# Optimization experiments

Hardware: AMD Instinct MI355X
Metric: run time of the kernel (lower is better)

Reference implementation:

```python
import jax, jax.numpy as jnp
import numpy as np

N_NEIGHBORS = 9
MIN_STD, MAX_STD = 0.01, 0.5
EPS = 1e-8


def setup_inputs() -> dict:
    key = jax.random.key(0)
    k1, k2, k3 = jax.random.split(key, 3)
    B, C, H, W = 8, 2048, 28, 28
    M = 8192
    features = jax.random.normal(k1, (B, C, H, W), dtype=jnp.float32)
    memory_bank = jax.random.normal(k2, (M, C), dtype=jnp.float32)
    influence_weight = jnp.ones((C,), dtype=jnp.float32)
    distance_weight = jnp.ones((1,), dtype=jnp.float32)
    noise_unit = jax.random.normal(k3, (B * H * W, C), dtype=jnp.float32)
    return {
        "features": features,
        "memory_bank": memory_bank,
        "influence_weight": influence_weight,
        "distance_weight": distance_weight,
        "noise_unit": noise_unit,
    }


def _std(x, axis=None, keepdims=False):
    # torch.std default: unbiased (ddof=1)
    return jnp.std(x, axis=axis, keepdims=keepdims, ddof=1)


def reference(features, memory_bank, influence_weight, distance_weight, noise_unit):
    B, C, H, W = features.shape
    M = memory_bank.shape[0]
    k = min(N_NEIGHBORS, M)

    # [B*H*W, C]
    f = features.transpose(0, 2, 3, 1).reshape(B * H * W, C)

    # Euclidean cdist via the (||a||^2 + ||b||^2 - 2 a.b) expansion
    f2 = jnp.sum(f * f, axis=1, keepdims=True)            # [N,1]
    m2 = jnp.sum(memory_bank * memory_bank, axis=1)       # [M]
    d2 = f2 + m2[None, :] - 2.0 * (f @ memory_bank.T)     # [N,M]
    dist = jnp.sqrt(jnp.clip(d2, 0.0, None))

    # top-k smallest distances (sorted ascending, like torch.topk largest=False)
    neg_vals, idx = jax.lax.top_k(-dist, k)               # [N,k]
    topk_distances = -neg_vals

    # gather neighbor features and per-dim influence
    nn_feats = memory_bank[idx]                           # [N,k,C]
    influence_scores = jnp.mean(jnp.abs(f[:, None, :] - nn_feats), axis=1)  # [N,C]
    influence_scores = influence_scores * influence_weight[None, :]

    # normalize influence per-row
    influence_norm = influence_scores - jnp.mean(influence_scores, axis=-1, keepdims=True)
    influence_norm = influence_norm / (_std(influence_scores, axis=-1, keepdims=True) + EPS)

    # distance signal: row-mean distance, broadcast to [N,C], global-normalized
    ds = jnp.mean(topk_distances, axis=-1, keepdims=True)  # [N,1]
    ds_e = jnp.broadcast_to(ds, influence_norm.shape)      # [N,C]
    distance_norm = (ds_e - jnp.mean(ds_e)) / (_std(ds_e) + EPS)

    combined = influence_norm + distance_weight * distance_norm
    noise_std = MIN_STD + (MAX_STD - MIN_STD) * jax.nn.sigmoid(combined)  # [N,C]

    noised_flat = f + noise_unit * noise_std
    noised_features = noised_flat.reshape(B, H, W, C).transpose(0, 3, 1, 2)
    influence_map = jnp.mean(influence_scores, axis=-1).reshape(B, H, W)
    noise_std_map = jnp.mean(noise_std, axis=-1).reshape(B, H, W)
    return noised_features, influence_map, noise_std_map
```

## Files before the change

### kernel.cpp

```cpp
#include <hip/hip_runtime.h>
#include <math.h>

typedef __attribute__((ext_vector_type(8))) __bf16 bf16x8;
typedef __attribute__((ext_vector_type(4))) float f32x4;

#define NB 8
#define NC 2048
#define NHW 784
#define NROWS 6272
#define NM 8192
#define NNEI 9
#define NCAND 12
#define NKT 64

static_assert(NROWS == NB * NHW, "dims");

__device__ __forceinline__ unsigned umin32(unsigned a, unsigned b) { return a < b ? a : b; }

__global__ __launch_bounds__(256) void prep_kernel(const float* __restrict__ feat,
                                                   const float* __restrict__ mb,
                                                   float* __restrict__ Af32,
                                                   __bf16* __restrict__ Ahi,
                                                   __bf16* __restrict__ Bhi,
                                                   float* __restrict__ m2) {
  int bid = blockIdx.x;
  int tid = threadIdx.x;
  if (bid < 12800) {
    __shared__ float tile[32][33];
    int b = bid / 1600;
    int c0 = ((bid / 25) & 63) * 32;
    int hw0 = (bid % 25) * 32;
    int tx = tid & 31, ty = tid >> 5;
#pragma unroll
    for (int i = 0; i < 4; ++i) {
      int c = c0 + ty + i * 8;
      int hw = hw0 + tx;
      float v = 0.f;
      if (hw < NHW) v = feat[((size_t)b * NC + c) * NHW + hw];
      tile[ty + i * 8][tx] = v;
    }
    __syncthreads();
#pragma unroll
    for (int i = 0; i < 4; ++i) {
      int hwl = ty + i * 8;
      int hw = hw0 + hwl;
      if (hw < NHW) {
        int n = b * NHW + hw;
        float v = tile[tx][hwl];
        Af32[(size_t)n * NC + c0 + tx] = v;
        Ahi[(size_t)n * NC + c0 + tx] = (__bf16)v;
      }
    }
  } else {
    __shared__ float red[4];
    int m = bid - 12800;
    float ss = 0.f;
#pragma unroll
    for (int i = 0; i < NC / 256; ++i) {
      int c = tid + i * 256;
      float v = mb[(size_t)m * NC + c];
      Bhi[(size_t)m * NC + c] = (__bf16)v;
      ss += v * v;
    }
#pragma unroll
    for (int off = 32; off; off >>= 1) ss += __shfl_xor(ss, off);
    if ((tid & 63) == 0) red[tid >> 6] = ss;
    __syncthreads();
    if (tid == 0) m2[m] = red[0] + red[1] + red[2] + red[3];
  }
}

#define STAGE(SRC, DST) \
  __builtin_amdgcn_global_load_lds((const __attribute__((address_space(1))) void*)(SRC), \
                                   (__attribute__((address_space(3))) void*)(DST), 16, 0, 0)

__global__ __launch_bounds__(512, 2) void gemm8_kernel(const __bf16* __restrict__ Ahi,
                                                       const __bf16* __restrict__ Bhi,
                                                       const float* __restrict__ m2,
                                                       unsigned short* __restrict__ dotq) {
  __shared__ __align__(16) char lds[131072];
  int tid = threadIdx.x;
  int lane = tid & 63, w = tid >> 6;
  int bid = blockIdx.x;
  int r = lane & 15, kq = lane >> 4;
  int r4 = (lane >> 4) * 4, cL = lane & 15;

  if (bid >= 768) {
    int lb = bid - 768;
    size_t m0l = (size_t)(lb & 7) * 1024 + (size_t)(lb >> 3) * 32;
    int n0l = 6144 + w * 16;
    const __bf16* aB = Ahi + (size_t)(n0l + r) * NC + kq * 8;
    const __bf16* bB0 = Bhi + (m0l + r) * NC + kq * 8;
    const __bf16* bB1 = Bhi + (m0l + 16 + r) * NC + kq * 8;
    f32x4 acc0 = {}, acc1 = {};
    bf16x8 a0 = *(const bf16x8*)aB;
    bf16x8 b0 = *(const bf16x8*)bB0;
    bf16x8 b1 = *(const bf16x8*)bB1;
#pragma unroll 4
    for (int kt = 0; kt < NKT; ++kt) {
      int ktn = (kt + 1) & 63;
      bf16x8 an = *(const bf16x8*)(aB + ktn * 32);
      bf16x8 b0n = *(const bf16x8*)(bB0 + ktn * 32);
      bf16x8 b1n = *(const bf16x8*)(bB1 + ktn * 32);
      acc0 = __builtin_amdgcn_mfma_f32_16x16x32_bf16(a0, b0, acc0, 0, 0, 0);
      acc1 = __builtin_amdgcn_mfma_f32_16x16x32_bf16(a0, b1, acc1, 0, 0, 0);
      a0 = an; b0 = b0n; b1 = b1n;
    }
#pragma unroll
    for (int g = 0; g < 2; ++g) {
      float m2g = m2[m0l + g * 16 + cL];
      f32x4 ac = g ? acc1 : acc0;
#pragma unroll
      for (int q = 0; q < 4; ++q) {
        int grow = n0l + r4 + q;
        float sc = m2g - 2.f * ac[q];
        int qi = (int)(sc * 16.f);
        qi = qi < 0 ? 0 : (qi > 65535 ? 65535 : qi);
        dotq[(size_t)grow * NM + (m0l + g * 16 + cL)] = (unsigned short)qi;
      }
    }
    return;
  }

  int xcd = bid & 7, lin = bid >> 3;
  int mt = xcd * 4 + (lin & 3), rtl = lin >> 2;
  size_t n0 = (size_t)rtl * 256, m0 = (size_t)mt * 256;
  int wr = w >> 2, wc = w & 3;

  int p = lane & 3;
  const char* aSrc[2];
  const char* bSrc[2];
  int aDst[2], bDst[2];
#pragma unroll
  for (int j = 0; j < 2; ++j) {
    int rloc = (w * 2 + j) * 16 + (lane >> 2);
    int kqs = (p - (rloc >> 1)) & 3;
    aSrc[j] = (const char*)Ahi + (n0 + rloc) * (NC * 2) + kqs * 16;
    bSrc[j] = (const char*)Bhi + (m0 + rloc) * (NC * 2) + kqs * 16;
    aDst[j] = (w * 2 + j) * 1024;
    bDst[j] = 16384 + (w * 2 + j) * 1024;
  }
  int s16 = (kq + (r >> 1)) & 3;
  int aRd = wr * 8192 + r * 64 + s16 * 16;
  int bRd = 16384 + wc * 4096 + r * 64 + s16 * 16;

  f32x4 acc[8][4] = {};

#pragma unroll
  for (int t = 0; t < 2; ++t) {
    int sb = t * 32768, kb = t * 64;
#pragma unroll
    for (int j = 0; j < 2; ++j)
      STAGE(aSrc[j] + kb, lds + sb + aDst[j]);
#pragma unroll
    for (int j = 0; j < 2; ++j)
      STAGE(bSrc[j] + kb, lds + sb + bDst[j]);
  }
  asm volatile("s_waitcnt vmcnt(4)" ::: "memory");
  __builtin_amdgcn_s_barrier();
  __builtin_amdgcn_sched_barrier(0);

#pragma unroll 4
  for (int kt = 0; kt < NKT; ++kt) {
    int sb = (kt & 3) * 32768;
    int kt2 = (kt + 2) & 63;
    int sb2 = (kt2 & 3) * 32768;
    int kb2 = kt2 * 64;
    bf16x8 av[4], bv[4];
#pragma unroll
    for (int j = 0; j < 2; ++j)
      STAGE(aSrc[j] + kb2, lds + sb2 + aDst[j]);
#pragma unroll
    for (int f = 0; f < 4; ++f) av[f] = *(const bf16x8*)(lds + sb + aRd + f * 1024);
#pragma unroll
    for (int g = 0; g < 4; ++g) bv[g] = *(const bf16x8*)(lds + sb + bRd + g * 1024);
    __builtin_amdgcn_s_setprio(1);
#pragma unroll
    for (int f = 0; f < 4; ++f)
#pragma unroll
      for (int g = 0; g < 4; ++g)
        acc[f][g] = __builtin_amdgcn_mfma_f32_16x16x32_bf16(av[f], bv[g], acc[f][g], 0, 0, 0);
    __builtin_amdgcn_s_setprio(0);
#pragma unroll
    for (int j = 0; j < 2; ++j)
      STAGE(bSrc[j] + kb2, lds + sb2 + bDst[j]);
#pragma unroll
    for (int f = 0; f < 4; ++f) av[f] = *(const bf16x8*)(lds + sb + aRd + (f + 4) * 1024);
    __builtin_amdgcn_s_setprio(1);
#pragma unroll
    for (int f = 0; f < 4; ++f)
#pragma unroll
      for (int g = 0; g < 4; ++g)
        acc[f + 4][g] = __builtin_amdgcn_mfma_f32_16x16x32_bf16(av[f], bv[g], acc[f + 4][g], 0, 0, 0);
    __builtin_amdgcn_s_setprio(0);
    asm volatile("s_waitcnt vmcnt(4)" ::: "memory");
    __builtin_amdgcn_s_barrier();
    __builtin_amdgcn_sched_barrier(0);
  }

  float m2r[4];
#pragma unroll
  for (int g = 0; g < 4; ++g) m2r[g] = m2[m0 + wc * 64 + g * 16 + cL];
#pragma unroll
  for (int f = 0; f < 8; ++f) {
    int grow0 = (int)n0 + wr * 128 + f * 16 + r4;
#pragma unroll
    for (int g = 0; g < 4; ++g) {
      size_t gcol = m0 + wc * 64 + g * 16 + cL;
#pragma unroll
      for (int q = 0; q < 4; ++q) {
        float sc = m2r[g] - 2.f * acc[f][g][q];
        int qi = (int)(sc * 16.f);
        qi = qi < 0 ? 0 : (qi > 65535 ? 65535 : qi);
        dotq[(size_t)(grow0 + q) * NM + gcol] = (unsigned short)qi;
      }
    }
  }
}

__global__ __launch_bounds__(256) void selres_kernel(const unsigned short* __restrict__ dotq,
                                                     const float* __restrict__ Af32,
                                                     const float* __restrict__ mb,
                                                     int* __restrict__ tki,
                                                     float* __restrict__ dsv) {
  __shared__ float fbuf[NC];
  __shared__ unsigned wmin[4];
  __shared__ int cidxL[NCAND];
  __shared__ double d2s[NCAND];
  int n = blockIdx.x;
  int tid = threadIdx.x;
  int lane = tid & 63, w = tid >> 6;

  unsigned kk[32];
  {
    const uint4* dq = (const uint4*)(dotq + (size_t)n * NM + tid * 32);
    unsigned base = tid * 32;
#pragma unroll
    for (int s = 0; s < 4; ++s) {
      uint4 v = dq[s];
      unsigned c0 = v.x, c1 = v.y, c2 = v.z, c3 = v.w;
      kk[s * 8 + 0] = ((c0 & 0xFFFFu) << 13) | (base + s * 8 + 0);
      kk[s * 8 + 1] = ((c0 >> 16) << 13)     | (base + s * 8 + 1);
      kk[s * 8 + 2] = ((c1 & 0xFFFFu) << 13) | (base + s * 8 + 2);
      kk[s * 8 + 3] = ((c1 >> 16) << 13)     | (base + s * 8 + 3);
      kk[s * 8 + 4] = ((c2 & 0xFFFFu) << 13) | (base + s * 8 + 4);
      kk[s * 8 + 5] = ((c2 >> 16) << 13)     | (base + s * 8 + 5);
      kk[s * 8 + 6] = ((c3 & 0xFFFFu) << 13) | (base + s * 8 + 6);
      kk[s * 8 + 7] = ((c3 >> 16) << 13)     | (base + s * 8 + 7);
    }
  }
#pragma unroll
  for (int i = 0; i < NC / 256; ++i)
    fbuf[tid + i * 256] = Af32[(size_t)n * NC + tid + i * 256];

  unsigned lmin = 0xFFFFFFFFu;
#pragma unroll
  for (int i = 0; i < 32; ++i) lmin = umin32(lmin, kk[i]);
  unsigned t = lmin;
#pragma unroll
  for (int off = 32; off; off >>= 1) t = umin32(t, (unsigned)__shfl_xor((int)t, off));
  if (lane == 0) wmin[w] = t;
  __syncthreads();

  for (int r = 0; r < NCAND; ++r) {
    unsigned g = umin32(umin32(wmin[0], wmin[1]), umin32(wmin[2], wmin[3]));
    if (tid == 0) cidxL[r] = (int)(g & 8191u);
    __syncthreads();
    int owner = (int)((g & 8191u) >> 5);
    if ((owner >> 6) == w) {
      if (tid == owner) {
#pragma unroll
        for (int i = 0; i < 32; ++i)
          if (kk[i] == g) kk[i] = 0xFFFFFFFFu;
        lmin = 0xFFFFFFFFu;
#pragma unroll
        for (int i = 0; i < 32; ++i) lmin = umin32(lmin, kk[i]);
      }
      unsigned t2 = lmin;
#pragma unroll
      for (int off = 32; off; off >>= 1) t2 = umin32(t2, (unsigned)__shfl_xor((int)t2, off));
      if (lane == 0) wmin[w] = t2;
    }
    __syncthreads();
  }

#pragma unroll
  for (int jj = 0; jj < 3; ++jj) {
    int j = w * 3 + jj;
    const float* mrow = mb + (size_t)cidxL[j] * NC;
    double acc = 0.0;
#pragma unroll
    for (int i = 0; i < 32; ++i) {
      int c = lane + i * 64;
      double d = (double)fbuf[c] - (double)mrow[c];
      acc += d * d;
    }
#pragma unroll
    for (int off = 32; off; off >>= 1) acc += __shfl_xor(acc, off);
    if (lane == 0) d2s[j] = acc;
  }
  __syncthreads();

  if (tid == 0) {
    double dacc = 0.0;
    bool used[NCAND] = {};
    for (int r = 0; r < NNEI; ++r) {
      int bj = 0; double bv = 1e300; int bidx = 0x7fffffff;
      for (int j = 0; j < NCAND; ++j) {
        if (used[j]) continue;
        if (d2s[j] < bv || (d2s[j] == bv && cidxL[j] < bidx)) { bv = d2s[j]; bidx = cidxL[j]; bj = j; }
      }
      used[bj] = true;
      tki[(size_t)n * NNEI + r] = bidx;
      dacc += sqrt(bv > 0.0 ? bv : 0.0);
    }
    dsv[n] = (float)(dacc * (1.0 / 9.0));
  }
}

__global__ __launch_bounds__(256) void stats_kernel(const float* __restrict__ dsv,
                                                    float* __restrict__ stats) {
  __shared__ float buf[NROWS];
  __shared__ float red[4];
  int tid = threadIdx.x;
  float s = 0.f;
  for (int i = tid; i < NROWS; i += 256) { float v = dsv[i]; buf[i] = v; s += v; }
#pragma unroll
  for (int off = 32; off; off >>= 1) s += __shfl_xor(s, off);
  if ((tid & 63) == 0) red[tid >> 6] = s;
  __syncthreads();
  float mu = (red[0] + red[1] + red[2] + red[3]) * (1.f / NROWS);
  __syncthreads();
  float q = 0.f;
  for (int i = tid; i < NROWS; i += 256) { float d = buf[i] - mu; q += d * d; }
#pragma unroll
  for (int off = 32; off; off >>= 1) q += __shfl_xor(q, off);
  if ((tid & 63) == 0) red[tid >> 6] = q;
  __syncthreads();
  if (tid == 0) {
    float SSb = (red[0] + red[1] + red[2] + red[3]) * (float)NC;
    float var = SSb / ((float)NROWS * (float)NC - 1.f);
    stats[0] = mu;
    stats[1] = 1.f / (sqrtf(var) + 1e-8f);
  }
}

__global__ __launch_bounds__(256) void fuse_kernel(const float* __restrict__ Af32,
                                                   const __bf16* __restrict__ Bhi,
                                                   const float* __restrict__ noise,
                                                   const float* __restrict__ iw,
                                                   const float* __restrict__ dwp,
                                                   const int* __restrict__ topk_idx,
                                                   const float* __restrict__ dsv,
                                                   const float* __restrict__ stats,
                                                   float* __restrict__ noised_tmp,
                                                   float* __restrict__ out_infl,
                                                   float* __restrict__ out_nstd) {
  __shared__ int idx[NNEI];
  __shared__ float red[4];
  int n = blockIdx.x;
  int tid = threadIdx.x;
  if (tid < NNEI) idx[tid] = topk_idx[(size_t)n * NNEI + tid];
  __syncthreads();

  int c0 = tid * 8;
  const float* frow = Af32 + (size_t)n * NC + c0;
  float4 fa = *(const float4*)frow;
  float4 fb = *(const float4*)(frow + 4);
  float f_c[8] = {fa.x, fa.y, fa.z, fa.w, fb.x, fb.y, fb.z, fb.w};
  float a_c[8] = {};
  for (int j = 0; j < NNEI; ++j) {
    bf16x8 mv = *(const bf16x8*)(Bhi + (size_t)idx[j] * NC + c0);
#pragma unroll
    for (int k = 0; k < 8; ++k) a_c[k] += fabsf(f_c[k] - (float)mv[k]);
  }
  float4 w0 = *(const float4*)(iw + c0);
  float4 w1 = *(const float4*)(iw + c0 + 4);
  float wv[8] = {w0.x, w0.y, w0.z, w0.w, w1.x, w1.y, w1.z, w1.w};
  float s_c[8];
  float sum_s = 0.f, sum_s2 = 0.f;
#pragma unroll
  for (int k = 0; k < 8; ++k) {
    float s = (a_c[k] * (1.f / 9.f)) * wv[k];
    s_c[k] = s;
    sum_s += s;
    sum_s2 += s * s;
  }
#pragma unroll
  for (int off = 32; off; off >>= 1) sum_s += __shfl_xor(sum_s, off);
  if ((tid & 63) == 0) red[tid >> 6] = sum_s;
  __syncthreads();
  float tot_s = red[0] + red[1] + red[2] + red[3];
  __syncthreads();
#pragma unroll
  for (int off = 32; off; off >>= 1) sum_s2 += __shfl_xor(sum_s2, off);
  if ((tid & 63) == 0) red[tid >> 6] = sum_s2;
  __syncthreads();
  float tot_s2 = red[0] + red[1] + red[2] + red[3];
  __syncthreads();

  float mu = tot_s * (1.f / NC);
  float var = (tot_s2 - (float)NC * mu * mu) * (1.f / (NC - 1));
  float rstd = 1.f / (sqrtf(fmaxf(var, 0.f)) + 1e-8f);
  float dnorm = (dsv[n] - stats[0]) * stats[1];
  float dwv = dwp[0];

  float4 na = *(const float4*)(noise + (size_t)n * NC + c0);
  float4 nb = *(const float4*)(noise + (size_t)n * NC + c0 + 4);
  float nz[8] = {na.x, na.y, na.z, na.w, nb.x, nb.y, nb.z, nb.w};
  float o[8];
  float nsum = 0.f;
#pragma unroll
  for (int k = 0; k < 8; ++k) {
    float inorm = (s_c[k] - mu) * rstd;
    float comb = inorm + dwv * dnorm;
    float sig = 1.f / (1.f + expf(-comb));
    float nstd = 0.01f + 0.49f * sig;
    nsum += nstd;
    o[k] = f_c[k] + nz[k] * nstd;
  }
  float* orow = noised_tmp + (size_t)n * NC + c0;
  *(float4*)orow = make_float4(o[0], o[1], o[2], o[3]);
  *(float4*)(orow + 4) = make_float4(o[4], o[5], o[6], o[7]);
#pragma unroll
  for (int off = 32; off; off >>= 1) nsum += __shfl_xor(nsum, off);
  if ((tid & 63) == 0) red[tid >> 6] = nsum;
  __syncthreads();
  if (tid == 0) {
    out_infl[n] = tot_s * (1.f / NC);
    out_nstd[n] = (red[0] + red[1] + red[2] + red[3]) * (1.f / NC);
  }
}

__global__ __launch_bounds__(256) void transpose_kernel(const float* __restrict__ src,
                                                        float* __restrict__ dst) {
  __shared__ float tile[32][33];
  int b = blockIdx.z;
  int c0 = blockIdx.y * 32;
  int hw0 = blockIdx.x * 32;
  int tx = threadIdx.x & 31, ty = threadIdx.x >> 5;
#pragma unroll
  for (int i = 0; i < 4; ++i) {
    int hw = hw0 + ty + i * 8;
    if (hw < NHW) tile[ty + i * 8][tx] = src[((size_t)(b * NHW + hw)) * NC + c0 + tx];
  }
  __syncthreads();
#pragma unroll
  for (int i = 0; i < 4; ++i) {
    int c = c0 + ty + i * 8;
    int hw = hw0 + tx;
    if (hw < NHW) dst[((size_t)b * NC + c) * NHW + hw] = tile[tx][ty + i * 8];
  }
}

extern "C" void kernel_launch(void* const* d_in, const int* in_sizes, int n_in,
                              void* d_out, int out_size, void* d_ws, size_t ws_size,
                              hipStream_t stream) {
  (void)in_sizes; (void)n_in; (void)out_size; (void)ws_size;
  const float* feat  = (const float*)d_in[0];
  const float* mb    = (const float*)d_in[1];
  const float* iw    = (const float*)d_in[2];
  const float* dwp   = (const float*)d_in[3];
  const float* noise = (const float*)d_in[4];
  float* out = (float*)d_out;
  float* out_noised = out;
  float* out_infl = out + (size_t)NB * NC * NHW;
  float* out_nstd = out_infl + NROWS;

  char* ws = (char*)d_ws;
  size_t off = 0;
  auto alloc = [&](size_t sz) -> char* {
    char* p = ws + off;
    off += (sz + 255) & ~(size_t)255;
    return p;
  };
  float* Af32 = (float*)alloc((size_t)NROWS * NC * 4);
  __bf16* Ahi = (__bf16*)alloc((size_t)NROWS * NC * 2);
  __bf16* Bhi = (__bf16*)alloc((size_t)NM * NC * 2);
  float* m2v = (float*)alloc((size_t)NM * 4);
  int* tki = (int*)alloc((size_t)NROWS * NNEI * 4);
  float* dsv = (float*)alloc((size_t)NROWS * 4);
  float* stv = (float*)alloc(256);
  unsigned short* dotq = (unsigned short*)alloc((size_t)NROWS * NM * 2);
  float* noised_tmp = (float*)dotq;

  prep_kernel<<<12800 + NM, 256, 0, stream>>>(feat, mb, Af32, Ahi, Bhi, m2v);
  gemm8_kernel<<<1024, 512, 0, stream>>>(Ahi, Bhi, m2v, dotq);
  selres_kernel<<<NROWS, 256, 0, stream>>>(dotq, Af32, mb, tki, dsv);
  stats_kernel<<<1, 256, 0, stream>>>(dsv, stv);
  fuse_kernel<<<NROWS, 256, 0, stream>>>(Af32, Bhi, noise, iw, dwp, tki, dsv, stv,
                                         noised_tmp, out_infl, out_nstd);
  transpose_kernel<<<dim3(25, 64, NB), 256, 0, stream>>>(noised_tmp, out_noised);
}
```

Before: 440.3 us.

## Switch distance GEMM to int8 MFMA with wider candidate re-rank

Quantizes features and memory bank to int8 (scale 20) and runs the candidate-distance GEMM with i32 16x16x64 int8 MFMA, halving the K-loop iterations and the bytes staged through LDS. To make up for the coarser screening, the exact double-precision re-rank now keeps 32 candidates instead of 12. This targets GEMM compute and bandwidth. It adds extra re-rank work and a separate int8 bank copy, and risks missing true neighbours when quantization error pushes them beyond the top 32. Clipping at ±127 (about ±6.35) is normally harmless for normal inputs.

```diff
diff --git a/kernel.cpp b/kernel.cpp
--- a/kernel.cpp
+++ b/kernel.cpp
@@ -3,6 +3,7 @@
 
 typedef __attribute__((ext_vector_type(8))) __bf16 bf16x8;
 typedef __attribute__((ext_vector_type(4))) float f32x4;
+typedef __attribute__((ext_vector_type(4))) int i32x4;
 
 #define NB 8
 #define NC 2048
@@ -10,17 +11,24 @@
 #define NROWS 6272
 #define NM 8192
 #define NNEI 9
-#define NCAND 12
-#define NKT 64
+#define NCAND 32
+#define NKT 32
 
 static_assert(NROWS == NB * NHW, "dims");
 
 __device__ __forceinline__ unsigned umin32(unsigned a, unsigned b) { return a < b ? a : b; }
+
+__device__ __forceinline__ signed char quant20(float v) {
+  int q = (int)rintf(v * 20.f);
+  q = q < -127 ? -127 : (q > 127 ? 127 : q);
+  return (signed char)q;
+}
 
 __global__ __launch_bounds__(256) void prep_kernel(const float* __restrict__ feat,
                                                    const float* __restrict__ mb,
                                                    float* __restrict__ Af32,
-                                                   __bf16* __restrict__ Ahi,
+                                                   signed char* __restrict__ Ai8,
+                                                   signed char* __restrict__ Bi8,
                                                    __bf16* __restrict__ Bhi,
                                                    float* __restrict__ m2) {
   int bid = blockIdx.x;
@@ -48,7 +56,7 @@
         int n = b * NHW + hw;
         float v = tile[tx][hwl];
         Af32[(size_t)n * NC + c0 + tx] = v;
-        Ahi[(size_t)n * NC + c0 + tx] = (__bf16)v;
+        Ai8[(size_t)n * NC + c0 + tx] = quant20(v);
       }
     }
   } else {
@@ -59,6 +67,7 @@
     for (int i = 0; i < NC / 256; ++i) {
       int c = tid + i * 256;
       float v = mb[(size_t)m * NC + c];
+      Bi8[(size_t)m * NC + c] = quant20(v);
       Bhi[(size_t)m * NC + c] = (__bf16)v;
       ss += v * v;
     }
@@ -74,8 +83,8 @@
   __builtin_amdgcn_global_load_lds((const __attribute__((address_space(1))) void*)(SRC), \
                                    (__attribute__((address_space(3))) void*)(DST), 16, 0, 0)
 
-__global__ __launch_bounds__(512, 2) void gemm8_kernel(const __bf16* __restrict__ Ahi,
-                                                       const __bf16* __restrict__ Bhi,
+__global__ __launch_bounds__(512, 2) void gemm8_kernel(const signed char* __restrict__ Ai8,
+                                                       const signed char* __restrict__ Bi8,
                                                        const float* __restrict__ m2,
                                                        unsigned short* __restrict__ dotq) {
   __shared__ __align__(16) char lds[131072];
@@ -89,32 +98,31 @@
     int lb = bid - 768;
     size_t m0l = (size_t)(lb & 7) * 1024 + (size_t)(lb >> 3) * 32;
     int n0l = 6144 + w * 16;
-    const __bf16* aB = Ahi + (size_t)(n0l + r) * NC + kq * 8;
-    const __bf16* bB0 = Bhi + (m0l + r) * NC + kq * 8;
-    const __bf16* bB1 = Bhi + (m0l + 16 + r) * NC + kq * 8;
-    f32x4 acc0 = {}, acc1 = {};
-    bf16x8 a0 = *(const bf16x8*)aB;
-    bf16x8 b0 = *(const bf16x8*)bB0;
-    bf16x8 b1 = *(const bf16x8*)bB1;
+    const signed char* aB = Ai8 + (size_t)(n0l + r) * NC + kq * 16;
+    const signed char* bB0 = Bi8 + (m0l + r) * NC + kq * 16;
+    const signed char* bB1 = Bi8 + (m0l + 16 + r) * NC + kq * 16;
+    i32x4 acc0 = {}, acc1 = {};
+    i32x4 a0 = *(const i32x4*)aB;
+    i32x4 b0 = *(const i32x4*)bB0;
+    i32x4 b1 = *(const i32x4*)bB1;
 #pragma unroll 4
     for (int kt = 0; kt < NKT; ++kt) {
-      int ktn = (kt + 1) & 63;
-      bf16x8 an = *(const bf16x8*)(aB + ktn * 32);
-      bf16x8 b0n = *(const bf16x8*)(bB0 + ktn * 32);
-      bf16x8 b1n = *(const bf16x8*)(bB1 + ktn * 32);
-      acc0 = __builtin_amdgcn_mfma_f32_16x16x32_bf16(a0, b0, acc0, 0, 0, 0);
-      acc1 = __builtin_amdgcn_mfma_f32_16x16x32_bf16(a0, b1, acc1, 0, 0, 0);
+      int ktn = (kt + 1) & 31;
+      i32x4 an = *(const i32x4*)(aB + ktn * 64);
+      i32x4 b0n = *(const i32x4*)(bB0 + ktn * 64);
+      i32x4 b1n = *(const i32x4*)(bB1 + ktn * 64);
+      acc0 = __builtin_amdgcn_mfma_i32_16x16x64_i8(a0, b0, acc0, 0, 0, 0);
+      acc1 = __builtin_amdgcn_mfma_i32_16x16x64_i8(a0, b1, acc1, 0, 0, 0);
       a0 = an; b0 = b0n; b1 = b1n;
     }
 #pragma unroll
     for (int g = 0; g < 2; ++g) {
-      float m2g = m2[m0l + g * 16 + cL];
-      f32x4 ac = g ? acc1 : acc0;
+      float m2g16 = m2[m0l + g * 16 + cL] * 16.f;
+      i32x4 ac = g ? acc1 : acc0;
 #pragma unroll
       for (int q = 0; q < 4; ++q) {
         int grow = n0l + r4 + q;
-        float sc = m2g - 2.f * ac[q];
-        int qi = (int)(sc * 16.f);
+        int qi = (int)(m2g16 - (float)ac[q] * 0.08f);
         qi = qi < 0 ? 0 : (qi > 65535 ? 65535 : qi);
         dotq[(size_t)grow * NM + (m0l + g * 16 + cL)] = (unsigned short)qi;
       }
@@ -135,8 +143,8 @@
   for (int j = 0; j < 2; ++j) {
     int rloc = (w * 2 + j) * 16 + (lane >> 2);
     int kqs = (p - (rloc >> 1)) & 3;
-    aSrc[j] = (const char*)Ahi + (n0 + rloc) * (NC * 2) + kqs * 16;
-    bSrc[j] = (const char*)Bhi + (m0 + rloc) * (NC * 2) + kqs * 16;
+    aSrc[j] = (const char*)Ai8 + (n0 + rloc) * NC + kqs * 16;
+    bSrc[j] = (const char*)Bi8 + (m0 + rloc) * NC + kqs * 16;
     aDst[j] = (w * 2 + j) * 1024;
     bDst[j] = 16384 + (w * 2 + j) * 1024;
   }
@@ -144,7 +152,7 @@
   int aRd = wr * 8192 + r * 64 + s16 * 16;
   int bRd = 16384 + wc * 4096 + r * 64 + s16 * 16;
 
-  f32x4 acc[8][4] = {};
+  i32x4 acc[8][4] = {};
 
 #pragma unroll
   for (int t = 0; t < 2; ++t) {
@@ -163,44 +171,44 @@
 #pragma unroll 4
   for (int kt = 0; kt < NKT; ++kt) {
     int sb = (kt & 3) * 32768;
-    int kt2 = (kt + 2) & 63;
+    int kt2 = (kt + 2) & 31;
     int sb2 = (kt2 & 3) * 32768;
     int kb2 = kt2 * 64;
-    bf16x8 av[4], bv[4];
+    i32x4 av[4], bv[4];
 #pragma unroll
     for (int j = 0; j < 2; ++j)
       STAGE(aSrc[j] + kb2, lds + sb2 + aDst[j]);
 #pragma unroll
-    for (int f = 0; f < 4; ++f) av[f] = *(const bf16x8*)(lds + sb + aRd + f * 1024);
-#pragma unroll
-    for (int g = 0; g < 4; ++g) bv[g] = *(const bf16x8*)(lds + sb + bRd + g * 1024);
+    for (int f = 0; f < 4; ++f) av[f] = *(const i32x4*)(lds + sb + aRd + f * 1024);
+#pragma unroll
+    for (int g = 0; g < 4; ++g) bv[g] = *(const i32x4*)(lds + sb + bRd + g * 1024);
     __builtin_amdgcn_s_setprio(1);
 #pragma unroll
     for (int f = 0; f < 4; ++f)
 #pragma unroll
       for (int g = 0; g < 4; ++g)
-        acc[f][g] = __builtin_amdgcn_mfma_f32_16x16x32_bf16(av[f], bv[g], acc[f][g], 0, 0, 0);
+        acc[f][g] = __builtin_amdgcn_mfma_i32_16x16x64_i8(av[f], bv[g], acc[f][g], 0, 0, 0);
     __builtin_amdgcn_s_setprio(0);
 #pragma unroll
     for (int j = 0; j < 2; ++j)
       STAGE(bSrc[j] + kb2, lds + sb2 + bDst[j]);
 #pragma unroll
-    for (int f = 0; f < 4; ++f) av[f] = *(const bf16x8*)(lds + sb + aRd + (f + 4) * 1024);
+    for (int f = 0; f < 4; ++f) av[f] = *(const i32x4*)(lds + sb + aRd + (f + 4) * 1024);
     __builtin_amdgcn_s_setprio(1);
 #pragma unroll
     for (int f = 0; f < 4; ++f)
 #pragma unroll
       for (int g = 0; g < 4; ++g)
-        acc[f + 4][g] = __builtin_amdgcn_mfma_f32_16x16x32_bf16(av[f], bv[g], acc[f + 4][g], 0, 0, 0);
+        acc[f + 4][g] = __builtin_amdgcn_mfma_i32_16x16x64_i8(av[f], bv[g], acc[f + 4][g], 0, 0, 0);
     __builtin_amdgcn_s_setprio(0);
     asm volatile("s_waitcnt vmcnt(4)" ::: "memory");
     __builtin_amdgcn_s_barrier();
     __builtin_amdgcn_sched_barrier(0);
   }
 
-  float m2r[4];
-#pragma unroll
-  for (int g = 0; g < 4; ++g) m2r[g] = m2[m0 + wc * 64 + g * 16 + cL];
+  float m2r16[4];
+#pragma unroll
+  for (int g = 0; g < 4; ++g) m2r16[g] = m2[m0 + wc * 64 + g * 16 + cL] * 16.f;
 #pragma unroll
   for (int f = 0; f < 8; ++f) {
     int grow0 = (int)n0 + wr * 128 + f * 16 + r4;
@@ -209,8 +217,7 @@
       size_t gcol = m0 + wc * 64 + g * 16 + cL;
 #pragma unroll
       for (int q = 0; q < 4; ++q) {
-        float sc = m2r[g] - 2.f * acc[f][g][q];
-        int qi = (int)(sc * 16.f);
+        int qi = (int)(m2r16[g] - (float)acc[f][g][q] * 0.08f);
         qi = qi < 0 ? 0 : (qi > 65535 ? 65535 : qi);
         dotq[(size_t)(grow0 + q) * NM + gcol] = (unsigned short)qi;
       }
@@ -285,8 +292,8 @@
   }
 
 #pragma unroll
-  for (int jj = 0; jj < 3; ++jj) {
-    int j = w * 3 + jj;
+  for (int jj = 0; jj < 8; ++jj) {
+    int j = w * 8 + jj;
     const float* mrow = mb + (size_t)cidxL[j] * NC;
     double acc = 0.0;
 #pragma unroll
@@ -475,7 +482,8 @@
     return p;
   };
   float* Af32 = (float*)alloc((size_t)NROWS * NC * 4);
-  __bf16* Ahi = (__bf16*)alloc((size_t)NROWS * NC * 2);
+  signed char* Ai8 = (signed char*)alloc((size_t)NROWS * NC);
+  signed char* Bi8 = (signed char*)alloc((size_t)NM * NC);
   __bf16* Bhi = (__bf16*)alloc((size_t)NM * NC * 2);
   float* m2v = (float*)alloc((size_t)NM * 4);
   int* tki = (int*)alloc((size_t)NROWS * NNEI * 4);
@@ -484,8 +492,8 @@
   unsigned short* dotq = (unsigned short*)alloc((size_t)NROWS * NM * 2);
   float* noised_tmp = (float*)dotq;
 
-  prep_kernel<<<12800 + NM, 256, 0, stream>>>(feat, mb, Af32, Ahi, Bhi, m2v);
-  gemm8_kernel<<<1024, 512, 0, stream>>>(Ahi, Bhi, m2v, dotq);
+  prep_kernel<<<12800 + NM, 256, 0, stream>>>(feat, mb, Af32, Ai8, Bi8, Bhi, m2v);
+  gemm8_kernel<<<1024, 512, 0, stream>>>(Ai8, Bi8, m2v, dotq);
   selres_kernel<<<NROWS, 256, 0, stream>>>(dotq, Af32, mb, tki, dsv);
   stats_kernel<<<1, 256, 0, stream>>>(dsv, stv);
   fuse_kernel<<<NROWS, 256, 0, stream>>>(Af32, Bhi, noise, iw, dwp, tki, dsv, stv,
```

Result: slower. 593.0 us (+34.7%).
